# Optimization experiments

Measured on AMD Instinct MI355X. Metric: run time of the kernel, lower is better.

The kernel has to match this reference:

```python
import jax, jax.numpy as jnp
import numpy as np

B, KVH, HPK, D = 4, 8, 4, 128          # batch, n_kv_heads, n_heads_per_kv, head_size
SEQ_KV = 4096                           # cached history length
SEQ = SEQ_KV + 1                        # history + current token
K, LOCAL_K, SINK, RANK = 512, 128, 4, 32


def gather(t, axis, i):
    """Broadcasting take_along_axis, mirroring the torch `gather` helper."""
    axis = axis % t.ndim
    tgt = list(t.shape)
    tgt[axis] = i.shape[axis]
    return jnp.take_along_axis(t, jnp.broadcast_to(i, tgt), axis)


def sparse_q_score(q, key_cpu_t, cur_key_t):
    # q: (B,KVH,HPK,1,D); key_cpu_t: (B,KVH,D,SEQ_KV); cur_key_t: (B,KVH,1,D,1)
    absq = jnp.abs(q).sum(2, keepdims=True)                    # (B,KVH,1,1,D)
    _, idx = jax.lax.top_k(absq, RANK)                         # (B,KVH,1,1,RANK)
    q_proj = gather(q, -1, idx)                                # (B,KVH,HPK,1,RANK)
    idx_t = jnp.swapaxes(idx, -1, -2)                          # (B,KVH,1,RANK,1)
    k_hist = gather(key_cpu_t[:, :, None], -2, idx_t)          # (B,KVH,1,RANK,SEQ_KV)
    k_cur = gather(cur_key_t, -2, idx_t)                       # (B,KVH,1,RANK,1)
    k_proj = jnp.concatenate([k_hist, k_cur], -1)              # (B,KVH,1,RANK,SEQ)
    scale = jnp.sqrt(jnp.abs(q_proj).sum(-1) / jnp.abs(q).sum(-1) * D)[..., None]
    return jnp.matmul(q_proj, k_proj) / scale                  # (B,KVH,HPK,1,SEQ)


def setup_inputs():
    key = jax.random.key(0)
    ks = jax.random.split(key, 6)
    query = jax.random.normal(ks[0], (B, KVH * HPK, 1, D), jnp.float32)
    k = jax.random.normal(ks[1], (B, KVH, 1, D), jnp.float32)
    v = jax.random.normal(ks[2], (B, KVH, 1, D), jnp.float32)
    logmask = jnp.zeros((B, KVH * HPK, 1, SEQ), jnp.float32)
    key_cpu = jax.random.normal(ks[3], (B, KVH, SEQ_KV, D), jnp.float32)
    value_cpu = jax.random.normal(ks[4], (B, KVH, SEQ_KV, D), jnp.float32)
    s_key_cpu = jnp.swapaxes(key_cpu, -1, -2)                  # head-size-contiguous copy
    mean_v = jax.random.normal(ks[5], (B, KVH, 1, 1, D), jnp.float32)
    return {"query": query, "key": k, "value": v, "logmask": logmask,
            "key_cpu": key_cpu, "value_cpu": value_cpu,
            "s_key_cpu": s_key_cpu, "mean_v": mean_v}


def reference(query, key, value, logmask, key_cpu, value_cpu, s_key_cpu, mean_v):
    q = query.reshape(B, KVH, HPK, 1, D)
    k = key.reshape(B, KVH, 1, 1, D)
    v = value.reshape(B, KVH, 1, 1, D)
    lm = logmask.reshape(B, KVH, HPK, 1, SEQ)
    # approximate scores over the full key history + current key
    score = (sparse_q_score(q, s_key_cpu, jnp.swapaxes(k, 3, 4)) + lm).astype(jnp.float32)
    # causal index over history (excluding current token): 0 = most recent unmasked
    neg = jnp.isneginf(lm[..., :-1])
    ci = jnp.where(neg, -1,
                   jnp.cumsum((~neg)[..., ::-1].astype(jnp.int32), -1)[..., ::-1] - 1)
    is_local = (0 <= ci) & (ci < LOCAL_K)
    is_sink = ci >= SEQ - SINK - 1
    fmax = jnp.finfo(jnp.float32).max
    topk_score = jnp.where(is_local | is_sink, fmax, score[..., :-1]).sum(2, keepdims=True)
    kk = min(K + SINK, SEQ)
    _, indices = jax.lax.top_k(topk_score, kk)                 # (B,KVH,1,1,kk)
    # running mean value update
    mean_v_new = (mean_v * (SEQ - 1) + v.astype(jnp.float32)) / SEQ
    # weight reallocation to the mean value
    norm = jax.nn.softmax(score, -1)
    kv_weight = gather(norm, -1, indices).sum(-1) + norm[..., -1]  # (B,KVH,HPK,1)
    # gather selected K/V and append current token
    kv_idx = indices[..., 0, :, None]                          # (B,KVH,1,kk,1)
    key_g = jnp.concatenate([gather(key_cpu[:, :, None], -2, kv_idx), k], -2)   # (B,KVH,1,kk+1,D)
    val_g = jnp.concatenate([gather(value_cpu[:, :, None], -2, kv_idx), v], -2)
    cur_idx = jnp.full(indices.shape[:-1] + (1,), SEQ - 1, indices.dtype)
    lm_g = gather(lm, -1, jnp.concatenate([indices, cur_idx], -1))  # (B,KVH,HPK,1,kk+1)
    # dense attention over the reduced key set
    scores = jnp.matmul(q, jnp.swapaxes(key_g, -1, -2)) * (D ** -0.5) + lm_g
    weights = jax.nn.softmax(scores.astype(jnp.float32), -1) * kv_weight[..., None]
    out = jnp.matmul(weights, val_g) + (1.0 - kv_weight[..., None]) * mean_v_new
    return out.reshape(B, KVH * HPK, 1, D), weights.reshape(B, KVH * HPK, 1, kk + 1)
```

## Files before the change

### kernel.cpp

```cpp
#include <hip/hip_runtime.h>
#include <hip/hip_bf16.h>
#include <math.h>

#define NBH 32
#define HPKN 4
#define DN 128
#define SEQKV 4096
#define SEQN 4097
#define SSTR 4100
#define RANKN 32
#define KSEL 516
#define SINKN 4
#define LOCALK 128
#define NMASK 132
#define NTOP 384

__global__ __launch_bounds__(256) void k2_scores(
    const float* __restrict__ q, const float* __restrict__ key,
    const float* __restrict__ skey, const float* __restrict__ lm,
    float* __restrict__ scores, float* __restrict__ tk) {
  int bh = blockIdx.y;
  int s0 = blockIdx.x << 9;
  int t = threadIdx.x;
  int wave = t >> 6, lane = t & 63;
  __shared__ float qv[4][128];
  __shared__ float absq[128];
  __shared__ int sel[RANKN];
  __shared__ float qp[4][RANKN];

  {
    float v0 = q[(size_t)bh * 512 + t];
    float v1 = q[(size_t)bh * 512 + 256 + t];
    qv[t >> 7][t & 127] = v0;
    qv[2 + (t >> 7)][t & 127] = v1;
  }
  __syncthreads();
  if (t < 128)
    absq[t] = fabsf(qv[0][t]) + fabsf(qv[1][t]) + fabsf(qv[2][t]) + fabsf(qv[3][t]);
  __syncthreads();
  if (t < 128) {
    float a = absq[t];
    int rank = 0;
    for (int e = 0; e < 128; ++e) {
      float ae = absq[e];
      rank += (ae > a) || (ae == a && e < t);
    }
    if (rank < RANKN) sel[rank] = t;
  }
  __syncthreads();
  {
    float fa = fabsf(qv[wave][lane]) + fabsf(qv[wave][lane + 64]);
    for (int off = 32; off > 0; off >>= 1) fa += __shfl_down(fa, off);
    float full = __shfl(fa, 0);
    float qsel = (lane < RANKN) ? qv[wave][sel[lane]] : 0.f;
    float sv = fabsf(qsel);
    for (int off = 32; off > 0; off >>= 1) sv += __shfl_down(sv, off);
    float selsum = __shfl(sv, 0);
    float scale = sqrtf(selsum / full * 128.f);
    if (lane < RANKN) qp[wave][lane] = qsel / scale;
  }
  __syncthreads();

  if (blockIdx.x == 0) {
    float kv = (lane < RANKN) ? key[bh * 128 + sel[lane]] : 0.f;
    float pr = (lane < RANKN) ? qp[wave][lane] * kv : 0.f;
    for (int off = 32; off > 0; off >>= 1) pr += __shfl_down(pr, off);
    if (lane == 0)
      scores[(size_t)(bh * 4 + wave) * SSTR + SEQKV] =
          pr + lm[(size_t)(bh * 4 + wave) * SEQN + SEQKV];
  }

  const float* kb = skey + (size_t)bh * 128 * 4096;
  float a00 = 0, a01 = 0, a02 = 0, a03 = 0;
  float a10 = 0, a11 = 0, a12 = 0, a13 = 0;
#pragma unroll 4
  for (int r = 0; r < RANKN; ++r) {
    const float* row = kb + ((size_t)sel[r] << 12) + s0;
    float k0 = row[t];
    float k1 = row[t + 256];
    float q0 = qp[0][r], q1 = qp[1][r], q2 = qp[2][r], q3 = qp[3][r];
    a00 += q0 * k0; a01 += q1 * k0; a02 += q2 * k0; a03 += q3 * k0;
    a10 += q0 * k1; a11 += q1 * k1; a12 += q2 * k1; a13 += q3 * k1;
  }
  float acc0[4] = {a00, a01, a02, a03};
  float acc1[4] = {a10, a11, a12, a13};
  {
    int s = s0 + t;
    float sum = 0;
    for (int p = 0; p < 4; ++p) {
      float sc = acc0[p] + lm[(size_t)(bh * 4 + p) * SEQN + s];
      scores[(size_t)(bh * 4 + p) * SSTR + s] = sc;
      sum += sc;
    }
    tk[(bh << 12) + s] = sum;
  }
  {
    int s = s0 + t + 256;
    float sum = 0;
    for (int p = 0; p < 4; ++p) {
      float sc = acc1[p] + lm[(size_t)(bh * 4 + p) * SEQN + s];
      scores[(size_t)(bh * 4 + p) * SSTR + s] = sc;
      sum += sc;
    }
    tk[(bh << 12) + s] = sum;
  }
}

__global__ __launch_bounds__(256) void k3_topk(
    const float* __restrict__ tk, int* __restrict__ indices) {
  int bh = blockIdx.x;
  int t = threadIdx.x;
  int lane = t & 63;
  __shared__ unsigned us[4096];
  __shared__ unsigned hist[2048];
  __shared__ unsigned long long binlist[2048];
  __shared__ unsigned long long selk[512];
  __shared__ unsigned chunkSum[32];
  __shared__ int c1, c2, binB_s, nAbove_s, needed_s;

  for (int s = t; s < 4096; s += 256) {
    unsigned b = __float_as_uint(tk[(bh << 12) + s]);
    us[s] = (b & 0x80000000u) ? ~b : (b | 0x80000000u);
  }
  for (int i = t; i < 2048; i += 256) hist[i] = 0;
  if (t == 0) { c1 = 0; c2 = 0; }
  __syncthreads();

  for (int s = SINKN + t; s < SEQKV - LOCALK; s += 256)
    atomicAdd(&hist[us[s] >> 21], 1u);
  __syncthreads();

  if (t < 32) {
    unsigned sum = 0;
    for (int i = 0; i < 64; ++i) sum += hist[t * 64 + i];
    chunkSum[t] = sum;
  }
  __syncthreads();

  if (t < 64) {
    int l = t;
    unsigned x = (l < 32) ? chunkSum[l] : 0;
    unsigned sfx = x;
    for (int off = 1; off < 64; off <<= 1) {
      unsigned y = __shfl_down(sfx, off);
      if (l + off < 64) sfx += y;
    }
    unsigned above = sfx - x;
    bool hit = (l < 32) && (above < NTOP) && (above + x >= NTOP);
    unsigned long long mask = __ballot(hit);
    int C = __ffsll(mask) - 1;
    unsigned aboveC = __shfl(above, C);
    unsigned h = hist[C * 64 + l];
    unsigned sfx2 = h;
    for (int off = 1; off < 64; off <<= 1) {
      unsigned y = __shfl_down(sfx2, off);
      if (l + off < 64) sfx2 += y;
    }
    unsigned above2 = aboveC + (sfx2 - h);
    bool hit2 = (above2 < NTOP) && (above2 + h >= NTOP);
    unsigned long long mask2 = __ballot(hit2);
    int lB = __ffsll(mask2) - 1;
    if (l == lB) {
      binB_s = C * 64 + l;
      nAbove_s = (int)above2;
      needed_s = NTOP - (int)above2;
    }
  }
  __syncthreads();
  unsigned B = (unsigned)binB_s;
  int nAbove = nAbove_s, needed = needed_s;

  for (int s0 = SINKN; s0 < SEQKV - LOCALK; s0 += 256) {
    int s = s0 + t;
    bool valid = (s < SEQKV - LOCALK);
    unsigned u = valid ? us[s] : 0u;
    unsigned bin = u >> 21;
    bool win = valid && (bin > B);
    bool bnd = valid && (bin == B);
    unsigned long long mw = __ballot(win);
    unsigned long long mb = __ballot(bnd);
    int bw = 0, bb = 0;
    if (lane == 0) {
      if (mw) bw = atomicAdd(&c1, __popcll(mw));
      if (mb) bb = atomicAdd(&c2, __popcll(mb));
    }
    bw = __shfl(bw, 0);
    bb = __shfl(bb, 0);
    unsigned long long lmask = (1ULL << lane) - 1ULL;
    unsigned long long key = ((unsigned long long)u << 32) | (unsigned)(~s);
    if (win) selk[bw + __popcll(mw & lmask)] = key;
    if (bnd) {
      int pos = bb + __popcll(mb & lmask);
      if (pos < 2048) binlist[pos] = key;
    }
  }
  __syncthreads();
  int m2 = c2;
  int p2 = 1;
  while (p2 < m2) p2 <<= 1;
  for (int i = m2 + t; i < p2; i += 256) binlist[i] = 0ULL;
  __syncthreads();
  for (int k = 2; k <= p2; k <<= 1)
    for (int j = k >> 1; j > 0; j >>= 1) {
      for (int i = t; i < p2; i += 256) {
        int ixj = i ^ j;
        if (ixj > i) {
          bool desc = ((i & k) == 0);
          unsigned long long a = binlist[i], bb2 = binlist[ixj];
          if ((a < bb2) == desc) { binlist[i] = bb2; binlist[ixj] = a; }
        }
      }
      __syncthreads();
    }
  for (int i = t; i < needed; i += 256) selk[nAbove + i] = binlist[i];
  for (int i = NTOP + t; i < 512; i += 256) selk[i] = 0ULL;
  __syncthreads();
  for (int k = 2; k <= 512; k <<= 1)
    for (int j = k >> 1; j > 0; j >>= 1) {
      for (int i = t; i < 512; i += 256) {
        int ixj = i ^ j;
        if (ixj > i) {
          bool desc = ((i & k) == 0);
          unsigned long long a = selk[i], bb2 = selk[ixj];
          if ((a < bb2) == desc) { selk[i] = bb2; selk[ixj] = a; }
        }
      }
      __syncthreads();
    }
  if (t < SINKN) indices[bh * KSEL + t] = t;
  for (int i = t; i < LOCALK; i += 256)
    indices[bh * KSEL + SINKN + i] = (SEQKV - LOCALK) + i;
  for (int i = t; i < NTOP; i += 256)
    indices[bh * KSEL + NMASK + i] = (int)(~(unsigned)(selk[i] & 0xFFFFFFFFu));
}

__global__ __launch_bounds__(256) void k5_qk(
    const float* __restrict__ q, const float* __restrict__ key,
    const float* __restrict__ lm, const float* __restrict__ key_cpu,
    const int* __restrict__ indices, float* __restrict__ s2_g) {
  int bh = blockIdx.y;
  int t = threadIdx.x;
  int wave = t >> 6, lane = t & 63;
  __shared__ float qs[512];
  __shared__ int sidx[KSEL];
  qs[t] = q[((size_t)bh * 4 << 7) + t];
  qs[t + 256] = q[((size_t)bh * 4 << 7) + t + 256];
  for (int j = t; j < KSEL; j += 256) sidx[j] = indices[bh * KSEL + j];
  __syncthreads();

  const float rsqd = 0.08838834764831845f;
  float q0a = qs[lane * 2], q0b = qs[lane * 2 + 1];
  float q1a = qs[128 + lane * 2], q1b = qs[128 + lane * 2 + 1];
  float q2a = qs[256 + lane * 2], q2b = qs[256 + lane * 2 + 1];
  float q3a = qs[384 + lane * 2], q3b = qs[384 + lane * 2 + 1];

  for (int i = 0; i < 10; ++i) {
    int j = (blockIdx.x << 2) + wave + 52 * i;
    if (j > KSEL) continue;
    int sj = (j < KSEL) ? sidx[j] : SEQKV;
    const float* krow = (j < KSEL)
        ? key_cpu + ((((size_t)bh << 12) + sj) << 7)
        : key + ((size_t)bh << 7);
    float2 kk = ((const float2*)krow)[lane];
    float p0 = q0a * kk.x + q0b * kk.y;
    float p1 = q1a * kk.x + q1b * kk.y;
    float p2 = q2a * kk.x + q2b * kk.y;
    float p3 = q3a * kk.x + q3b * kk.y;
    for (int off = 32; off > 0; off >>= 1) {
      p0 += __shfl_down(p0, off);
      p1 += __shfl_down(p1, off);
      p2 += __shfl_down(p2, off);
      p3 += __shfl_down(p3, off);
    }
    if (lane == 0) {
      size_t lmb = (size_t)bh * 4 * SEQN + sj;
      s2_g[(bh * 4 + 0) * 520 + j] = p0 * rsqd + lm[lmb + 0 * SEQN];
      s2_g[(bh * 4 + 1) * 520 + j] = p1 * rsqd + lm[lmb + 1 * SEQN];
      s2_g[(bh * 4 + 2) * 520 + j] = p2 * rsqd + lm[lmb + 2 * SEQN];
      s2_g[(bh * 4 + 3) * 520 + j] = p3 * rsqd + lm[lmb + 3 * SEQN];
    }
  }
}

__global__ __launch_bounds__(256) void k6_stats(
    const float* __restrict__ scores, const int* __restrict__ indices,
    const float* __restrict__ s2_g, const float* __restrict__ value,
    const float* __restrict__ mean_v,
    float* __restrict__ out_w, float* __restrict__ w_g,
    float* __restrict__ out) {
  int bhp = blockIdx.x;
  int bh = bhp >> 2;
  int t = threadIdx.x;
  __shared__ int sidx[KSEL];
  __shared__ float red[256];
  __shared__ float bc;

  for (int j = t; j < KSEL; j += 256) sidx[j] = indices[bh * KSEL + j];
  __syncthreads();

  const float* srow = scores + (size_t)bhp * SSTR;
  const float4* srow4 = (const float4*)srow;
  float mx = -INFINITY;
  for (int i = t; i < 1024; i += 256) {
    float4 v = srow4[i];
    mx = fmaxf(mx, fmaxf(fmaxf(v.x, v.y), fmaxf(v.z, v.w)));
  }
  if (t == 0) mx = fmaxf(mx, srow[SEQKV]);
  red[t] = mx; __syncthreads();
  for (int st = 128; st > 0; st >>= 1) {
    if (t < st) red[t] = fmaxf(red[t], red[t + st]);
    __syncthreads();
  }
  float m = red[0]; __syncthreads();
  float se = 0.f;
  for (int i = t; i < 1024; i += 256) {
    float4 v = srow4[i];
    se += expf(v.x - m) + expf(v.y - m) + expf(v.z - m) + expf(v.w - m);
  }
  if (t == 0) se += expf(srow[SEQKV] - m);
  red[t] = se; __syncthreads();
  for (int st = 128; st > 0; st >>= 1) {
    if (t < st) red[t] += red[t + st];
    __syncthreads();
  }
  float sumexp = red[0]; __syncthreads();
  float ss = 0.f;
  for (int j = t; j < KSEL; j += 256) ss += expf(srow[sidx[j]] - m);
  red[t] = ss; __syncthreads();
  for (int st = 128; st > 0; st >>= 1) {
    if (t < st) red[t] += red[t + st];
    __syncthreads();
  }
  float kvw;
  if (t == 0) bc = (red[0] + expf(srow[SEQKV] - m)) / sumexp;
  __syncthreads();
  kvw = bc; __syncthreads();

  const float* s2r = s2_g + (size_t)bhp * 520;
  float mx2 = -INFINITY;
  for (int j = t; j < KSEL + 1; j += 256) mx2 = fmaxf(mx2, s2r[j]);
  red[t] = mx2; __syncthreads();
  for (int st = 128; st > 0; st >>= 1) {
    if (t < st) red[t] = fmaxf(red[t], red[t + st]);
    __syncthreads();
  }
  float m2 = red[0]; __syncthreads();
  float se2 = 0.f;
  for (int j = t; j < KSEL + 1; j += 256) se2 += expf(s2r[j] - m2);
  red[t] = se2; __syncthreads();
  for (int st = 128; st > 0; st >>= 1) {
    if (t < st) red[t] += red[t + st];
    __syncthreads();
  }
  float inv = kvw / red[0];

  for (int j = t; j < KSEL + 1; j += 256) {
    float w = expf(s2r[j] - m2) * inv;
    out_w[(size_t)bhp * (KSEL + 1) + j] = w;
    w_g[(size_t)bhp * 520 + j] = w;
  }

  if (t < 128) {
    float vcur = value[((size_t)bh << 7) + t];
    float mvn = (mean_v[((size_t)bh << 7) + t] * 4096.f + vcur) / 4097.f;
    out[((size_t)bhp << 7) + t] = (1.f - kvw) * mvn;
  }
}

__global__ __launch_bounds__(256) void k7_wv(
    const float* __restrict__ value, const float* __restrict__ value_cpu,
    const int* __restrict__ indices, const float* __restrict__ w_g,
    float* __restrict__ out) {
  int bh = blockIdx.y;
  int c0 = blockIdx.x << 6;
  int t = threadIdx.x;
  int d = t & 127, half = t >> 7;
  __shared__ int sidx[64];
  __shared__ float wsh[4][64];
  __shared__ float red[2][4][128];

  int nj = min(64, KSEL + 1 - c0);
  if (t < nj) {
    int j = c0 + t;
    sidx[t] = (j < KSEL) ? indices[bh * KSEL + j] : -1;
  }
  for (int i = t; i < 4 * 64; i += 256) {
    int p = i >> 6, jl = i & 63;
    wsh[p][jl] = (jl < nj) ? w_g[(size_t)(bh * 4 + p) * 520 + c0 + jl] : 0.f;
  }
  __syncthreads();

  float a0 = 0, a1 = 0, a2 = 0, a3 = 0;
  for (int jl = half; jl < nj; jl += 2) {
    int sj = sidx[jl];
    const float* vrow = (sj >= 0)
        ? value_cpu + ((((size_t)bh << 12) + sj) << 7)
        : value + ((size_t)bh << 7);
    float v = vrow[d];
    a0 += wsh[0][jl] * v;
    a1 += wsh[1][jl] * v;
    a2 += wsh[2][jl] * v;
    a3 += wsh[3][jl] * v;
  }
  red[half][0][d] = a0; red[half][1][d] = a1;
  red[half][2][d] = a2; red[half][3][d] = a3;
  __syncthreads();
  if (half == 0) {
#pragma unroll
    for (int p = 0; p < 4; ++p) {
      float s = red[0][p][d] + red[1][p][d];
      atomicAdd(&out[(size_t)(bh * 4 + p) * 128 + d], s);
    }
  }
}

extern "C" void kernel_launch(void* const* d_in, const int* in_sizes, int n_in,
                              void* d_out, int out_size, void* d_ws, size_t ws_size,
                              hipStream_t stream) {
  const float* query     = (const float*)d_in[0];
  const float* key       = (const float*)d_in[1];
  const float* value     = (const float*)d_in[2];
  const float* logmask   = (const float*)d_in[3];
  const float* key_cpu   = (const float*)d_in[4];
  const float* value_cpu = (const float*)d_in[5];
  const float* s_key_cpu = (const float*)d_in[6];
  const float* mean_v    = (const float*)d_in[7];

  float* out   = (float*)d_out;
  float* out_w = out + 16384;

  char* ws = (char*)d_ws;
  int*   indices   = (int*)(ws + 20480);
  float* scores    = (float*)(ws + 86528);
  float* tk        = (float*)(ws + 2185728);
  float* s2_g      = (float*)(ws + 2710016);
  float* w_g       = (float*)(ws + 2976256);

  hipLaunchKernelGGL(k2_scores, dim3(8, NBH), dim3(256), 0, stream,
                     query, key, s_key_cpu, logmask, scores, tk);
  hipLaunchKernelGGL(k3_topk, dim3(NBH), dim3(256), 0, stream,
                     tk, indices);
  hipLaunchKernelGGL(k5_qk, dim3(13, NBH), dim3(256), 0, stream,
                     query, key, logmask, key_cpu, indices, s2_g);
  hipLaunchKernelGGL(k6_stats, dim3(128), dim3(256), 0, stream,
                     scores, indices, s2_g, value, mean_v, out_w, w_g, out);
  hipLaunchKernelGGL(k7_wv, dim3(9, NBH), dim3(256), 0, stream,
                     value, value_cpu, indices, w_g, out);
}
```

Before: 248.5 us.

## Fuse softmax max/sum partials into score kernel and register-resident bitonic sort

The score kernel now computes per-block partial max and sum-of-exp for each head and writes them to a small partials buffer. The stats kernel combines these eight partials with an online-softmax merge instead of rereading the full 4097-wide score row twice. Separately, the final 512-element bitonic sort in top-k keeps elements in registers and uses wave shuffles for small strides, touching shared memory only for large strides. This cuts global memory passes and barriers, but adds exp work and two extra block syncs to the score kernel.

```diff
diff --git a/kernel.cpp b/kernel.cpp
--- a/kernel.cpp
+++ b/kernel.cpp
@@ -18,7 +18,8 @@
 __global__ __launch_bounds__(256) void k2_scores(
     const float* __restrict__ q, const float* __restrict__ key,
     const float* __restrict__ skey, const float* __restrict__ lm,
-    float* __restrict__ scores, float* __restrict__ tk) {
+    float* __restrict__ scores, float* __restrict__ tk,
+    float2* __restrict__ partials) {
   int bh = blockIdx.y;
   int s0 = blockIdx.x << 9;
   int t = threadIdx.x;
@@ -27,6 +28,7 @@
   __shared__ float absq[128];
   __shared__ int sel[RANKN];
   __shared__ float qp[4][RANKN];
+  __shared__ float wred[4][4];
 
   {
     float v0 = q[(size_t)bh * 512 + t];
@@ -82,13 +84,15 @@
     a00 += q0 * k0; a01 += q1 * k0; a02 += q2 * k0; a03 += q3 * k0;
     a10 += q0 * k1; a11 += q1 * k1; a12 += q2 * k1; a13 += q3 * k1;
   }
-  float acc0[4] = {a00, a01, a02, a03};
-  float acc1[4] = {a10, a11, a12, a13};
+  float sc0[4] = {a00, a01, a02, a03};
+  float sc1[4] = {a10, a11, a12, a13};
   {
     int s = s0 + t;
     float sum = 0;
+#pragma unroll
     for (int p = 0; p < 4; ++p) {
-      float sc = acc0[p] + lm[(size_t)(bh * 4 + p) * SEQN + s];
+      float sc = sc0[p] + lm[(size_t)(bh * 4 + p) * SEQN + s];
+      sc0[p] = sc;
       scores[(size_t)(bh * 4 + p) * SSTR + s] = sc;
       sum += sc;
     }
@@ -97,12 +101,38 @@
   {
     int s = s0 + t + 256;
     float sum = 0;
+#pragma unroll
     for (int p = 0; p < 4; ++p) {
-      float sc = acc1[p] + lm[(size_t)(bh * 4 + p) * SEQN + s];
+      float sc = sc1[p] + lm[(size_t)(bh * 4 + p) * SEQN + s];
+      sc1[p] = sc;
       scores[(size_t)(bh * 4 + p) * SSTR + s] = sc;
       sum += sc;
     }
     tk[(bh << 12) + s] = sum;
+  }
+
+#pragma unroll
+  for (int p = 0; p < 4; ++p) {
+    float mx = fmaxf(sc0[p], sc1[p]);
+    for (int off = 32; off > 0; off >>= 1) mx = fmaxf(mx, __shfl_down(mx, off));
+    if (lane == 0) wred[wave][p] = mx;
+  }
+  __syncthreads();
+  float bm[4];
+#pragma unroll
+  for (int p = 0; p < 4; ++p)
+    bm[p] = fmaxf(fmaxf(wred[0][p], wred[1][p]), fmaxf(wred[2][p], wred[3][p]));
+  __syncthreads();
+#pragma unroll
+  for (int p = 0; p < 4; ++p) {
+    float e = expf(sc0[p] - bm[p]) + expf(sc1[p] - bm[p]);
+    for (int off = 32; off > 0; off >>= 1) e += __shfl_down(e, off);
+    if (lane == 0) wred[wave][p] = e;
+  }
+  __syncthreads();
+  if (t < 4) {
+    float s = wred[0][t] + wred[1][t] + wred[2][t] + wred[3][t];
+    partials[(size_t)(bh * 4 + t) * 8 + blockIdx.x] = make_float2(bm[t], s);
   }
 }
 
@@ -215,23 +245,39 @@
   for (int i = t; i < needed; i += 256) selk[nAbove + i] = binlist[i];
   for (int i = NTOP + t; i < 512; i += 256) selk[i] = 0ULL;
   __syncthreads();
-  for (int k = 2; k <= 512; k <<= 1)
+
+  unsigned long long e0 = selk[t], e1 = selk[t + 256];
+  int i1 = t + 256;
+  for (int k = 2; k <= 512; k <<= 1) {
     for (int j = k >> 1; j > 0; j >>= 1) {
-      for (int i = t; i < 512; i += 256) {
-        int ixj = i ^ j;
-        if (ixj > i) {
-          bool desc = ((i & k) == 0);
-          unsigned long long a = selk[i], bb2 = selk[ixj];
-          if ((a < bb2) == desc) { selk[i] = bb2; selk[ixj] = a; }
-        }
+      if (j == 256) {
+        if (e0 < e1) { unsigned long long tmp = e0; e0 = e1; e1 = tmp; }
+      } else if (j >= 64) {
+        selk[t] = e0; selk[i1] = e1;
+        __syncthreads();
+        unsigned long long p0 = selk[t ^ j], p1 = selk[i1 ^ j];
+        __syncthreads();
+        bool d0 = ((t & k) == 0), l0 = ((t & j) == 0);
+        e0 = (d0 == l0) ? (e0 > p0 ? e0 : p0) : (e0 < p0 ? e0 : p0);
+        bool d1 = ((i1 & k) == 0), l1 = ((i1 & j) == 0);
+        e1 = (d1 == l1) ? (e1 > p1 ? e1 : p1) : (e1 < p1 ? e1 : p1);
+      } else {
+        unsigned long long p0 = __shfl_xor(e0, j);
+        unsigned long long p1 = __shfl_xor(e1, j);
+        bool d0 = ((t & k) == 0), l0 = ((t & j) == 0);
+        e0 = (d0 == l0) ? (e0 > p0 ? e0 : p0) : (e0 < p0 ? e0 : p0);
+        bool d1 = ((i1 & k) == 0);
+        e1 = (d1 == l0) ? (e1 > p1 ? e1 : p1) : (e1 < p1 ? e1 : p1);
       }
-      __syncthreads();
-    }
+    }
+  }
+
   if (t < SINKN) indices[bh * KSEL + t] = t;
   for (int i = t; i < LOCALK; i += 256)
     indices[bh * KSEL + SINKN + i] = (SEQKV - LOCALK) + i;
-  for (int i = t; i < NTOP; i += 256)
-    indices[bh * KSEL + NMASK + i] = (int)(~(unsigned)(selk[i] & 0xFFFFFFFFu));
+  indices[bh * KSEL + NMASK + t] = (int)(~(unsigned)(e0 & 0xFFFFFFFFu));
+  if (t < NTOP - 256)
+    indices[bh * KSEL + NMASK + 256 + t] = (int)(~(unsigned)(e1 & 0xFFFFFFFFu));
 }
 
 __global__ __launch_bounds__(256) void k5_qk(
@@ -283,9 +329,9 @@
 }
 
 __global__ __launch_bounds__(256) void k6_stats(
-    const float* __restrict__ scores, const int* __restrict__ indices,
-    const float* __restrict__ s2_g, const float* __restrict__ value,
-    const float* __restrict__ mean_v,
+    const float* __restrict__ scores, const float2* __restrict__ partials,
+    const int* __restrict__ indices, const float* __restrict__ s2_g,
+    const float* __restrict__ value, const float* __restrict__ mean_v,
     float* __restrict__ out_w, float* __restrict__ w_g,
     float* __restrict__ out) {
   int bhp = blockIdx.x;
@@ -299,31 +345,22 @@
   __syncthreads();
 
   const float* srow = scores + (size_t)bhp * SSTR;
-  const float4* srow4 = (const float4*)srow;
-  float mx = -INFINITY;
-  for (int i = t; i < 1024; i += 256) {
-    float4 v = srow4[i];
-    mx = fmaxf(mx, fmaxf(fmaxf(v.x, v.y), fmaxf(v.z, v.w)));
-  }
-  if (t == 0) mx = fmaxf(mx, srow[SEQKV]);
-  red[t] = mx; __syncthreads();
-  for (int st = 128; st > 0; st >>= 1) {
-    if (t < st) red[t] = fmaxf(red[t], red[t + st]);
-    __syncthreads();
-  }
-  float m = red[0]; __syncthreads();
-  float se = 0.f;
-  for (int i = t; i < 1024; i += 256) {
-    float4 v = srow4[i];
-    se += expf(v.x - m) + expf(v.y - m) + expf(v.z - m) + expf(v.w - m);
-  }
-  if (t == 0) se += expf(srow[SEQKV] - m);
-  red[t] = se; __syncthreads();
-  for (int st = 128; st > 0; st >>= 1) {
-    if (t < st) red[t] += red[t + st];
-    __syncthreads();
-  }
-  float sumexp = red[0]; __syncthreads();
+  float cur = srow[SEQKV];
+
+  float m = cur, sumexp;
+  {
+    float2 pc[8];
+#pragma unroll
+    for (int c = 0; c < 8; ++c) {
+      pc[c] = partials[(size_t)bhp * 8 + c];
+      m = fmaxf(m, pc[c].x);
+    }
+    float s = expf(cur - m);
+#pragma unroll
+    for (int c = 0; c < 8; ++c) s += pc[c].y * expf(pc[c].x - m);
+    sumexp = s;
+  }
+
   float ss = 0.f;
   for (int j = t; j < KSEL; j += 256) ss += expf(srow[sidx[j]] - m);
   red[t] = ss; __syncthreads();
@@ -332,7 +369,7 @@
     __syncthreads();
   }
   float kvw;
-  if (t == 0) bc = (red[0] + expf(srow[SEQKV] - m)) / sumexp;
+  if (t == 0) bc = (red[0] + expf(cur - m)) / sumexp;
   __syncthreads();
   kvw = bc; __syncthreads();
 
@@ -430,20 +467,22 @@
   float* out_w = out + 16384;
 
   char* ws = (char*)d_ws;
-  int*   indices   = (int*)(ws + 20480);
-  float* scores    = (float*)(ws + 86528);
-  float* tk        = (float*)(ws + 2185728);
-  float* s2_g      = (float*)(ws + 2710016);
-  float* w_g       = (float*)(ws + 2976256);
+  int*    indices  = (int*)(ws + 20480);
+  float*  scores   = (float*)(ws + 86528);
+  float*  tk       = (float*)(ws + 2185728);
+  float*  s2_g     = (float*)(ws + 2710016);
+  float*  w_g      = (float*)(ws + 2976256);
+  float2* partials = (float2*)(ws + 3242496);
 
   hipLaunchKernelGGL(k2_scores, dim3(8, NBH), dim3(256), 0, stream,
-                     query, key, s_key_cpu, logmask, scores, tk);
+                     query, key, s_key_cpu, logmask, scores, tk, partials);
   hipLaunchKernelGGL(k3_topk, dim3(NBH), dim3(256), 0, stream,
                      tk, indices);
   hipLaunchKernelGGL(k5_qk, dim3(13, NBH), dim3(256), 0, stream,
                      query, key, logmask, key_cpu, indices, s2_g);
   hipLaunchKernelGGL(k6_stats, dim3(128), dim3(256), 0, stream,
-                     scores, indices, s2_g, value, mean_v, out_w, w_g, out);
+                     scores, partials, indices, s2_g, value, mean_v,
+                     out_w, w_g, out);
   hipLaunchKernelGGL(k7_wv, dim3(9, NBH), dim3(256), 0, stream,
                      value, value_cpu, indices, w_g, out);
 }
```

Result: faster. 241.9 us (-2.7%).
